# Optimization experiments

Measured on AMD Instinct MI355X. Metric: run time of the kernel, lower is better.

## Reference

```python
import jax, jax.numpy as jnp
import numpy as np

N_HEAD = 16
ROPE_BASE = 10000.0


def _rope_tables(T, head_dim, dtype=jnp.float32):
    inv_freq = 1.0 / (ROPE_BASE ** (jnp.arange(0, head_dim, 2, dtype=jnp.float32) / head_dim))
    t = jnp.arange(T, dtype=jnp.float32)
    freqs = t[:, None] * inv_freq[None, :]          # [T, D/2]
    emb = jnp.concatenate([freqs, freqs], axis=-1)  # [T, D]
    return jnp.cos(emb).astype(dtype), jnp.sin(emb).astype(dtype)


def _rotate_half(x):
    d = x.shape[-1] // 2
    return jnp.concatenate([-x[..., d:], x[..., :d]], axis=-1)


def setup_inputs() -> dict:
    key = jax.random.key(0)
    ks = jax.random.split(key, 5)
    B, T, C = 2, 2048, 2048
    s = 1.0 / np.sqrt(C)
    return {
        "x": jax.random.normal(ks[0], (B, T, C), dtype=jnp.float32),
        "wq": jax.random.normal(ks[1], (C, C), dtype=jnp.float32) * s,
        "wk": jax.random.normal(ks[2], (C, C), dtype=jnp.float32) * s,
        "wv": jax.random.normal(ks[3], (C, C), dtype=jnp.float32) * s,
        "wo": jax.random.normal(ks[4], (C, C), dtype=jnp.float32) * s,
    }


def reference(x, wq, wk, wv, wo):
    B, T, C = x.shape
    H = N_HEAD
    D = C // H

    def heads(y):  # [B,T,C] -> [B,H,T,D]
        return y.reshape(B, T, H, D).transpose(0, 2, 1, 3)

    q = heads(x @ wq)
    k = heads(x @ wk)
    v = heads(x @ wv)

    cos, sin = _rope_tables(T, D, x.dtype)          # [T, D]
    cos = cos[None, None, :, :]
    sin = sin[None, None, :, :]
    q = q * cos + _rotate_half(q) * sin
    k = k * cos + _rotate_half(k) * sin

    scale = 1.0 / np.sqrt(D)
    scores = jnp.einsum('bhqd,bhkd->bhqk', q, k) * scale   # [B,H,T,T]
    causal = jnp.tril(jnp.ones((T, T), dtype=bool))
    scores = jnp.where(causal[None, None, :, :], scores, jnp.finfo(scores.dtype).min)
    attn = jax.nn.softmax(scores, axis=-1)
    y = jnp.einsum('bhqk,bhkd->bhqd', attn, v)             # [B,H,T,D]
    y = y.transpose(0, 2, 1, 3).reshape(B, T, C)
    return y @ wo
```

## Files before the change

kernel.cpp:

```cpp
#include <hip/hip_runtime.h>
#include <hip/hip_bf16.h>
#include <math.h>


#define TT 2048
#define CCn 2048
#define HH 16
#define DD 128
#define MMr 4096
#define NQKV 6144

typedef __attribute__((ext_vector_type(8))) short s16x8;
typedef __attribute__((ext_vector_type(4))) short s16x4;
typedef __attribute__((ext_vector_type(4))) float f32x4;

__device__ __forceinline__ short bf16_of(float f) {
  unsigned u = __float_as_uint(f);
  unsigned r = u + 0x7fffu + ((u >> 16) & 1u);
  return (short)(r >> 16);
}
__device__ __forceinline__ float f_of_bf16(short s) {
  return __uint_as_float(((unsigned)(unsigned short)s) << 16);
}
__device__ __forceinline__ float ex2(float x) { return exp2f(x); }

__device__ __forceinline__ void lds_load16(const void* g, void* l) {
  __builtin_amdgcn_global_load_lds((__attribute__((address_space(1))) void*)g,
                                   (__attribute__((address_space(3))) void*)l,
                                   16, 0, 0);
}

__global__ __launch_bounds__(256) void k_tables(float* __restrict__ cosT,
                                                float* __restrict__ sinT) {
  int idx = blockIdx.x * 256 + threadIdx.x;
  int t = idx >> 6, i = idx & 63;
  float inv = powf(10000.0f, -(float)i * (1.0f / 64.0f));
  float f = (float)t * inv;
  cosT[idx] = cosf(f);
  sinT[idx] = sinf(f);
}

__global__ __launch_bounds__(256) void k_cast_x(const float* __restrict__ x,
                                                short* __restrict__ xb) {
  int i = blockIdx.x * 256 + threadIdx.x;
  f32x4 v = ((const f32x4*)x)[i];
  s16x4 o;
#pragma unroll
  for (int j = 0; j < 4; ++j) o[j] = bf16_of(v[j]);
  ((s16x4*)xb)[i] = o;
}

__global__ __launch_bounds__(256) void k_wtrans(const float* __restrict__ w,
                                                short* __restrict__ wt) {
  __shared__ float tile[32][33];
  int n0 = blockIdx.x * 32, k0 = blockIdx.y * 32;
  int tx = threadIdx.x & 31, ty = threadIdx.x >> 5;
#pragma unroll
  for (int j = 0; j < 4; ++j) {
    int k = ty * 4 + j;
    tile[k][tx] = w[(size_t)(k0 + k) * CCn + n0 + tx];
  }
  __syncthreads();
#pragma unroll
  for (int j = 0; j < 4; ++j) {
    int n = ty * 4 + j;
    wt[(size_t)(n0 + n) * CCn + k0 + tx] = bf16_of(tile[tx][n]);
  }
}

__global__ __launch_bounds__(256) void k_vtrans(const short* __restrict__ src,
                                                short* __restrict__ dst) {
  __shared__ short tile[32][33];
  int bh = blockIdx.y, b = bh >> 4, h = bh & 15;
  int dt = blockIdx.x & 3, tt = blockIdx.x >> 2;
  int tx = threadIdx.x & 31, ty = threadIdx.x >> 5;
  const short* sp = src + ((size_t)(b * TT + tt * 32)) * NQKV + 4096 + h * DD + dt * 32;
#pragma unroll
  for (int j = 0; j < 4; ++j) {
    int tr = ty * 4 + j;
    tile[tr][tx] = sp[(size_t)tr * NQKV + tx];
  }
  __syncthreads();
  short* dp = dst + ((size_t)(bh * DD + dt * 32)) * TT + tt * 32;
#pragma unroll
  for (int j = 0; j < 4; ++j) {
    int dr = ty * 4 + j;
    dp[(size_t)dr * TT + tx] = tile[tx][dr];
  }
}

__global__ __launch_bounds__(256) void k_rope(const short* __restrict__ qkv, int coff,
                                              const float* __restrict__ cosT,
                                              const float* __restrict__ sinT,
                                              short* __restrict__ dst, float mul) {
  int idx = blockIdx.x * 256 + threadIdx.x;
  int i4 = (idx & 15) * 4;
  int h = (idx >> 4) & 15;
  int t = (idx >> 8) & 2047;
  int b = idx >> 19;
  const short* row = qkv + ((size_t)(b * TT + t)) * NQKV + coff + h * DD;
  s16x4 v0 = *(const s16x4*)(row + i4);
  s16x4 v1 = *(const s16x4*)(row + i4 + 64);
  f32x4 c4 = *(const f32x4*)(cosT + t * 64 + i4);
  f32x4 s4 = *(const f32x4*)(sinT + t * 64 + i4);
  s16x4 o0, o1;
#pragma unroll
  for (int j = 0; j < 4; ++j) {
    float a = f_of_bf16(v0[j]), bb = f_of_bf16(v1[j]);
    o0[j] = bf16_of((a * c4[j] - bb * s4[j]) * mul);
    o1[j] = bf16_of((bb * c4[j] + a * s4[j]) * mul);
  }
  short* orow = dst + ((size_t)((b * HH + h) * TT + t)) * DD;
  *(s16x4*)(orow + i4) = o0;
  *(s16x4*)(orow + i4 + 64) = o1;
}

template <bool BF16OUT>
__global__ __launch_bounds__(512, 2) void k_gemm256(const short* __restrict__ A,
                                                    const short* __restrict__ Bt,
                                                    void* __restrict__ Cout,
                                                    int M, int N, int K) {
  __shared__ short smem[65536];
  const int tid = threadIdx.x, wid = tid >> 6, lane = tid & 63;
  const int wm = wid >> 2, wn = wid & 3;
  const int lr = lane & 15, lk = lane >> 4;
  const int swz = (lk ^ ((lr >> 1) & 3)) * 8;

  int nwg = gridDim.x, orig = blockIdx.x;
  int xcd = orig & 7, idx = orig >> 3;
  int q = nwg >> 3, rmd = nwg & 7;
  int wg = (xcd < rmd) ? (xcd * (q + 1) + idx)
                       : (rmd * (q + 1) + (xcd - rmd) * q + idx);
  const int NBM = M >> 8;
  const int m0 = (wg % NBM) * 256, n0 = (wg / NBM) * 256;

  const int ldsbase = (tid & ~63);

  auto stageHalf = [&](const short* src, int r0, int slot, int kt, int h) {
#pragma unroll
    for (int l = 0; l < 2; ++l) {
      int lin = l * 512 + tid;
      int rr = lin >> 2, cs = lin & 3;
      int cc = cs ^ ((rr >> 1) & 3);
      lds_load16(src + (size_t)(r0 + rr) * K + kt * 64 + h * 32 + cc * 8,
                 smem + slot + (l * 512 + ldsbase) * 8);
    }
  };
  f32x4 acc[8][4] = {};
  s16x8 af[4], bfr[4];

  const int nk = K >> 6;
  stageHalf(A, m0, 0, 0, 0);
  stageHalf(Bt, n0, 32768, 0, 0);
  stageHalf(A, m0, 8192, 0, 1);
  stageHalf(Bt, n0, 32768 + 8192, 0, 1);
  stageHalf(A, m0, 16384, 1, 0);
  stageHalf(Bt, n0, 32768 + 16384, 1, 0);
  asm volatile("s_waitcnt vmcnt(4)" ::: "memory");
  __builtin_amdgcn_s_barrier();

#define PHASE_MFMA(mh)                                                        \
  __builtin_amdgcn_s_setprio(1);                                              \
  _Pragma("unroll") for (int i = 0; i < 4; ++i)                               \
      _Pragma("unroll") for (int j = 0; j < 4; ++j)                           \
      acc[(mh)*4 + i][j] = __builtin_amdgcn_mfma_f32_16x16x32_bf16(           \
          af[i], bfr[j], acc[(mh)*4 + i][j], 0, 0, 0);                        \
  __builtin_amdgcn_s_setprio(0);

#define LOAD_A(mh, ks, abuf)                                                  \
  _Pragma("unroll") for (int i = 0; i < 4; ++i)                               \
      af[i] = *(const s16x8*)(smem + (abuf)*16384 + (ks)*8192 +               \
                              (wm * 128 + (mh)*64 + i * 16 + lr) * 32 + swz);
#define LOAD_B(ks, abuf)                                                      \
  _Pragma("unroll") for (int j = 0; j < 4; ++j)                               \
      bfr[j] = *(const s16x8*)(smem + 32768 + (abuf)*16384 + (ks)*8192 +      \
                               (wn * 64 + j * 16 + lr) * 32 + swz);

#pragma unroll 1
  for (int kt = 0; kt < nk; ++kt) {
    const int buf = kt & 1, nbuf = buf ^ 1;
    const bool s1 = (kt + 1 < nk), s2 = (kt + 2 < nk);
    LOAD_B(0, buf);
    LOAD_A(0, 0, buf);
    if (s1) stageHalf(A, m0, nbuf * 16384 + 8192, kt + 1, 1);
    __builtin_amdgcn_s_barrier();
    PHASE_MFMA(0);
    __builtin_amdgcn_s_barrier();
    LOAD_A(1, 0, buf);
    if (s1) stageHalf(Bt, n0, 32768 + nbuf * 16384 + 8192, kt + 1, 1);
    __builtin_amdgcn_s_barrier();
    PHASE_MFMA(1);
    __builtin_amdgcn_s_barrier();
    LOAD_B(1, buf);
    LOAD_A(0, 1, buf);
    if (s2) stageHalf(A, m0, buf * 16384, kt + 2, 0);
    __builtin_amdgcn_s_barrier();
    PHASE_MFMA(0);
    __builtin_amdgcn_s_barrier();
    LOAD_A(1, 1, buf);
    if (s2) stageHalf(Bt, n0, 32768 + buf * 16384, kt + 2, 0);
    __builtin_amdgcn_s_barrier();
    PHASE_MFMA(1);
    asm volatile("s_waitcnt vmcnt(4)" ::: "memory");
    __builtin_amdgcn_s_barrier();
  }
#undef PHASE_MFMA
#undef LOAD_A
#undef LOAD_B

#pragma unroll
  for (int fi = 0; fi < 8; ++fi)
#pragma unroll
    for (int j = 0; j < 4; ++j) {
      int row = m0 + wm * 128 + (fi >> 2) * 64 + (fi & 3) * 16 + lk * 4;
      int col = n0 + wn * 64 + j * 16 + lr;
#pragma unroll
      for (int rr = 0; rr < 4; ++rr) {
        if (BF16OUT)
          ((short*)Cout)[(size_t)(row + rr) * N + col] = bf16_of(acc[fi][j][rr]);
        else
          ((float*)Cout)[(size_t)(row + rr) * N + col] = acc[fi][j][rr];
      }
    }
}

__global__ __launch_bounds__(256) void k_attn(const short* __restrict__ Qb,
                                              const short* __restrict__ Kb,
                                              const short* __restrict__ Vt,
                                              short* __restrict__ yb) {
  __shared__ short Ks[2][64 * 128];
  __shared__ short Vs[128 * 64];
  __shared__ short Ps[4][16 * 72];
  const int tid = threadIdx.x, wid = tid >> 6, lane = tid & 63;
  const int lr = lane & 15, lk = lane >> 4;
  const int bh = blockIdx.y, bx = blockIdx.x;
  const size_t baseQK = (size_t)bh * TT * DD;
  const int b = bh >> 4, h = bh & 15;

  auto stageK = [&](int bi, int kt2) {
#pragma unroll
    for (int it = 0; it < 4; ++it) {
      int ch = it * 256 + tid;
      int r = ch >> 4, cc = ch & 15;
      int cs = cc ^ (r & 7);
      lds_load16(Kb + baseQK + (size_t)(kt2 * 64 + r) * DD + cs * 8,
                 &Ks[bi][(size_t)(it * 256 + wid * 64) * 8]);
    }
  };
  auto stageV = [&](int kt2) {
#pragma unroll
    for (int it = 0; it < 4; ++it) {
      int ch = it * 256 + tid;
      int d = ch >> 3, kc = ch & 7;
      int cs = kc ^ (d & 7);
      lds_load16(Vt + baseQK + (size_t)d * TT + kt2 * 64 + cs * 8,
                 &Vs[(size_t)(it * 256 + wid * 64) * 8]);
    }
  };

#pragma unroll 1
  for (int pass = 0; pass < 2; ++pass) {
    const int qt = pass ? (31 - bx) : bx;
    const int q0 = qt * 64;
    const int qg = q0 + wid * 16 + lr;
    s16x8 qf[4];
#pragma unroll
    for (int ds = 0; ds < 4; ++ds)
      qf[ds] = *(const s16x8*)(Qb + baseQK + (size_t)qg * DD + (ds * 4 + lk) * 8);

    float mrun = -3.0e38f, lrun = 0.f;
    f32x4 yacc[8] = {};

    const int nkt = qt + 1;
    stageK(0, 0);
    stageV(0);
    __syncthreads();
    int buf = 0;
#pragma unroll 1
    for (int kt = 0; kt < nkt; ++kt) {
      if (kt + 1 < nkt) stageK(buf ^ 1, kt + 1);
      f32x4 sf[4] = {};
#pragma unroll
      for (int sub = 0; sub < 4; ++sub) {
        int kr = sub * 16 + lr;
#pragma unroll
        for (int ds = 0; ds < 4; ++ds) {
          int cc = (ds * 4 + lk) ^ (kr & 7);
          s16x8 kf = *(const s16x8*)(&Ks[buf][kr * 128 + cc * 8]);
          sf[sub] = __builtin_amdgcn_mfma_f32_16x16x32_bf16(kf, qf[ds], sf[sub], 0, 0, 0);
        }
      }
      const int kvbase = kt * 64;
      if (kvbase + 63 > q0 + wid * 16) {
#pragma unroll
        for (int sub = 0; sub < 4; ++sub)
#pragma unroll
          for (int r = 0; r < 4; ++r) {
            int kv = kvbase + sub * 16 + lk * 4 + r;
            if (kv > qg) sf[sub][r] = -3.0e38f;
          }
      }
      float tmax = -3.0e38f;
#pragma unroll
      for (int sub = 0; sub < 4; ++sub)
#pragma unroll
        for (int r = 0; r < 4; ++r) tmax = fmaxf(tmax, sf[sub][r]);
      tmax = fmaxf(tmax, __shfl_xor(tmax, 16, 64));
      tmax = fmaxf(tmax, __shfl_xor(tmax, 32, 64));
      if (!__all(tmax <= mrun + 11.0f)) {
        float mnew = fmaxf(mrun, tmax);
        float alpha = ex2(mrun - mnew);
        mrun = mnew;
        lrun *= alpha;
        float ar[4];
#pragma unroll
        for (int r = 0; r < 4; ++r) ar[r] = __shfl(alpha, lk * 4 + r, 64);
#pragma unroll
        for (int dn = 0; dn < 8; ++dn)
#pragma unroll
          for (int r = 0; r < 4; ++r) yacc[dn][r] *= ar[r];
      }
      float psum = 0.f;
#pragma unroll
      for (int sub = 0; sub < 4; ++sub) {
        s16x4 pq;
#pragma unroll
        for (int r = 0; r < 4; ++r) {
          float p = ex2(sf[sub][r] - mrun);
          psum += p;
          pq[r] = bf16_of(p);
        }
        *(s16x4*)(&Ps[wid][lr * 72 + sub * 16 + lk * 4]) = pq;
      }
      psum += __shfl_xor(psum, 16, 64);
      psum += __shfl_xor(psum, 32, 64);
      lrun += psum;
      __syncthreads();
      s16x8 pf0 = *(const s16x8*)(&Ps[wid][lr * 72 + lk * 8]);
      s16x8 pf1 = *(const s16x8*)(&Ps[wid][lr * 72 + 32 + lk * 8]);
#pragma unroll
      for (int dn = 0; dn < 8; ++dn) {
        int d = dn * 16 + lr;
        s16x8 vf0 = *(const s16x8*)(&Vs[d * 64 + (lk ^ (d & 7)) * 8]);
        yacc[dn] = __builtin_amdgcn_mfma_f32_16x16x32_bf16(pf0, vf0, yacc[dn], 0, 0, 0);
        s16x8 vf1 = *(const s16x8*)(&Vs[d * 64 + ((4 + lk) ^ (d & 7)) * 8]);
        yacc[dn] = __builtin_amdgcn_mfma_f32_16x16x32_bf16(pf1, vf1, yacc[dn], 0, 0, 0);
      }
      __syncthreads();
      if (kt + 1 < nkt) stageV(kt + 1);
      buf ^= 1;
    }
    float linv = 1.f / lrun;
    float lr4[4];
#pragma unroll
    for (int r = 0; r < 4; ++r) lr4[r] = __shfl(linv, lk * 4 + r, 64);
#pragma unroll
    for (int dn = 0; dn < 8; ++dn)
#pragma unroll
      for (int r = 0; r < 4; ++r) {
        int t = q0 + wid * 16 + lk * 4 + r;
        int c = h * DD + dn * 16 + lr;
        yb[((size_t)(b * TT + t)) * CCn + c] = bf16_of(yacc[dn][r] * lr4[r]);
      }
  }
}

extern "C" void kernel_launch(void* const* d_in, const int* in_sizes, int n_in,
                              void* d_out, int out_size, void* d_ws, size_t ws_size,
                              hipStream_t stream) {
  const float* x = (const float*)d_in[0];
  const float* wq = (const float*)d_in[1];
  const float* wk = (const float*)d_in[2];
  const float* wv = (const float*)d_in[3];
  const float* wo = (const float*)d_in[4];
  float* out = (float*)d_out;
  char* ws = (char*)d_ws;

  short* xb = (short*)(ws + 0);
  short* wqkvT = (short*)(ws + 16777216);
  short* woT = (short*)(ws + 41943040);
  short* qkv = (short*)(ws + 50331648);
  short* yb = (short*)(ws + 50331648);
  short* Qb = (short*)(ws + 100663296);
  short* Kb = (short*)(ws + 117440512);
  short* Vt = (short*)(ws + 134217728);
  float* cosT = (float*)(ws + 150994944);
  float* sinT = (float*)(ws + 151519232);

  const float kmul = 1.4426950408889634f / sqrtf(128.0f);

  k_tables<<<512, 256, 0, stream>>>(cosT, sinT);
  k_cast_x<<<8192, 256, 0, stream>>>(x, xb);
  k_wtrans<<<dim3(64, 64), 256, 0, stream>>>(wq, wqkvT);
  k_wtrans<<<dim3(64, 64), 256, 0, stream>>>(wk, wqkvT + (size_t)2048 * 2048);
  k_wtrans<<<dim3(64, 64), 256, 0, stream>>>(wv, wqkvT + (size_t)4096 * 2048);
  k_wtrans<<<dim3(64, 64), 256, 0, stream>>>(wo, woT);

  k_gemm256<true><<<16 * 24, 512, 0, stream>>>(xb, wqkvT, qkv, MMr, NQKV, CCn);

  k_rope<<<4096, 256, 0, stream>>>(qkv, 0, cosT, sinT, Qb, 1.0f);
  k_rope<<<4096, 256, 0, stream>>>(qkv, 2048, cosT, sinT, Kb, kmul);
  k_vtrans<<<dim3(256, 32), 256, 0, stream>>>(qkv, Vt);

  k_attn<<<dim3(16, 32), 256, 0, stream>>>(Qb, Kb, Vt, yb);

  k_gemm256<false><<<16 * 8, 512, 0, stream>>>(yb, woT, out, MMr, CCn, CCn);
}
```

Measured before the change: 425.9 us.

## Retile GEMMs to 128xBN blocks and merge weight-transpose and rope launches

Replaces the 256x256 GEMM tile with a templated 128-row by BN-column tile: 128x384 for the QKV projection and 128x256 for the output projection. This raises the workgroup count from 384/128 to 512/256 so the GPU's CUs are better filled, at the cost of less data reuse per block. It also fuses the four weight-transpose launches into one 3D-grid launch and the two rope launches into one, to cut launch overhead. The per-block LDS footprint and register count change, which alters occupancy.

```diff
diff --git a/kernel.cpp b/kernel.cpp
--- a/kernel.cpp
+++ b/kernel.cpp
@@ -50,9 +50,16 @@
   ((s16x4*)xb)[i] = o;
 }
 
-__global__ __launch_bounds__(256) void k_wtrans(const float* __restrict__ w,
-                                                short* __restrict__ wt) {
+__global__ __launch_bounds__(256) void k_wtrans4(const float* __restrict__ w0,
+                                                 const float* __restrict__ w1,
+                                                 const float* __restrict__ w2,
+                                                 const float* __restrict__ w3,
+                                                 short* __restrict__ wqkvT,
+                                                 short* __restrict__ woT) {
   __shared__ float tile[32][33];
+  int z = blockIdx.z;
+  const float* w = (z == 0) ? w0 : (z == 1) ? w1 : (z == 2) ? w2 : w3;
+  short* wt = (z == 3) ? woT : wqkvT + (size_t)z * 2048 * 2048;
   int n0 = blockIdx.x * 32, k0 = blockIdx.y * 32;
   int tx = threadIdx.x & 31, ty = threadIdx.x >> 5;
 #pragma unroll
@@ -89,10 +96,15 @@
   }
 }
 
-__global__ __launch_bounds__(256) void k_rope(const short* __restrict__ qkv, int coff,
-                                              const float* __restrict__ cosT,
-                                              const float* __restrict__ sinT,
-                                              short* __restrict__ dst, float mul) {
+__global__ __launch_bounds__(256) void k_rope2(const short* __restrict__ qkv,
+                                               const float* __restrict__ cosT,
+                                               const float* __restrict__ sinT,
+                                               short* __restrict__ Qb,
+                                               short* __restrict__ Kb, float kmul) {
+  int which = blockIdx.y;
+  int coff = which << 11;
+  short* dstb = which ? Kb : Qb;
+  float mul = which ? kmul : 1.0f;
   int idx = blockIdx.x * 256 + threadIdx.x;
   int i4 = (idx & 15) * 4;
   int h = (idx >> 4) & 15;
@@ -110,116 +122,134 @@
     o0[j] = bf16_of((a * c4[j] - bb * s4[j]) * mul);
     o1[j] = bf16_of((bb * c4[j] + a * s4[j]) * mul);
   }
-  short* orow = dst + ((size_t)((b * HH + h) * TT + t)) * DD;
+  short* orow = dstb + ((size_t)((b * HH + h) * TT + t)) * DD;
   *(s16x4*)(orow + i4) = o0;
   *(s16x4*)(orow + i4 + 64) = o1;
 }
 
-template <bool BF16OUT>
-__global__ __launch_bounds__(512, 2) void k_gemm256(const short* __restrict__ A,
-                                                    const short* __restrict__ Bt,
-                                                    void* __restrict__ Cout,
-                                                    int M, int N, int K) {
-  __shared__ short smem[65536];
+template <int BF, int BSTG, bool BF16OUT>
+__global__ __launch_bounds__(512) void k_gemmW(const short* __restrict__ A,
+                                               const short* __restrict__ Bt,
+                                               void* __restrict__ Cout,
+                                               int M, int N, int K) {
+  constexpr int BN = BF * 64;
+  constexpr int AH = 4096;
+  constexpr int BH = BN * 32;
+  __shared__ short smem[4 * AH + 4 * BH];
   const int tid = threadIdx.x, wid = tid >> 6, lane = tid & 63;
   const int wm = wid >> 2, wn = wid & 3;
   const int lr = lane & 15, lk = lane >> 4;
   const int swz = (lk ^ ((lr >> 1) & 3)) * 8;
 
   int nwg = gridDim.x, orig = blockIdx.x;
-  int xcd = orig & 7, idx = orig >> 3;
+  int xcd = orig & 7, bidx = orig >> 3;
   int q = nwg >> 3, rmd = nwg & 7;
-  int wg = (xcd < rmd) ? (xcd * (q + 1) + idx)
-                       : (rmd * (q + 1) + (xcd - rmd) * q + idx);
-  const int NBM = M >> 8;
-  const int m0 = (wg % NBM) * 256, n0 = (wg / NBM) * 256;
-
-  const int ldsbase = (tid & ~63);
-
-  auto stageHalf = [&](const short* src, int r0, int slot, int kt, int h) {
-#pragma unroll
-    for (int l = 0; l < 2; ++l) {
+  int wg = (xcd < rmd) ? (xcd * (q + 1) + bidx)
+                       : (rmd * (q + 1) + (xcd - rmd) * q + bidx);
+  const int NBM = M >> 7;
+  const int m0 = (wg % NBM) * 128, n0 = (wg / NBM) * BN;
+
+  const int ldswave = (tid & ~63) * 8;
+
+  auto stageA = [&](int buf, int h, int kt) {
+    int rr = tid >> 2, cs = tid & 3;
+    int cc = cs ^ ((rr >> 1) & 3);
+    lds_load16(A + (size_t)(m0 + rr) * K + kt * 64 + h * 32 + cc * 8,
+               smem + buf * 2 * AH + h * AH + ldswave);
+  };
+  auto stageB = [&](int buf, int h, int kt) {
+#pragma unroll
+    for (int l = 0; l < BSTG; ++l) {
       int lin = l * 512 + tid;
       int rr = lin >> 2, cs = lin & 3;
       int cc = cs ^ ((rr >> 1) & 3);
-      lds_load16(src + (size_t)(r0 + rr) * K + kt * 64 + h * 32 + cc * 8,
-                 smem + slot + (l * 512 + ldsbase) * 8);
+      lds_load16(Bt + (size_t)(n0 + rr) * K + kt * 64 + h * 32 + cc * 8,
+                 smem + 4 * AH + buf * 2 * BH + h * BH + l * 4096 + ldswave);
     }
   };
-  f32x4 acc[8][4] = {};
-  s16x8 af[4], bfr[4];
+
+  s16x8 af[4], bfr[BF / 2];
+  f32x4 acc[4][BF] = {};
+
+#define LOAD_A(ks, buf)                                                        \
+  _Pragma("unroll") for (int i = 0; i < 4; ++i) af[i] =                        \
+      *(const s16x8*)(smem + (buf) * 2 * AH + (ks) * AH +                      \
+                      (wm * 64 + i * 16 + lr) * 32 + swz);
+#define LOAD_B(ks, bh, buf)                                                    \
+  _Pragma("unroll") for (int j = 0; j < BF / 2; ++j) bfr[j] =                  \
+      *(const s16x8*)(smem + 4 * AH + (buf) * 2 * BH + (ks) * BH +             \
+                      (wn * (BF * 16) + ((bh) * (BF / 2) + j) * 16 + lr) * 32 +\
+                      swz);
+#define PHASE_MFMA(bh)                                                         \
+  __builtin_amdgcn_s_setprio(1);                                               \
+  _Pragma("unroll") for (int i = 0; i < 4; ++i)                                \
+      _Pragma("unroll") for (int j = 0; j < BF / 2; ++j)                       \
+      acc[i][(bh) * (BF / 2) + j] = __builtin_amdgcn_mfma_f32_16x16x32_bf16(   \
+          af[i], bfr[j], acc[i][(bh) * (BF / 2) + j], 0, 0, 0);                \
+  __builtin_amdgcn_s_setprio(0);
+#define VMCNT_N()                                                              \
+  if constexpr (BSTG == 3) asm volatile("s_waitcnt vmcnt(4)" ::: "memory");    \
+  else asm volatile("s_waitcnt vmcnt(3)" ::: "memory");
 
   const int nk = K >> 6;
-  stageHalf(A, m0, 0, 0, 0);
-  stageHalf(Bt, n0, 32768, 0, 0);
-  stageHalf(A, m0, 8192, 0, 1);
-  stageHalf(Bt, n0, 32768 + 8192, 0, 1);
-  stageHalf(A, m0, 16384, 1, 0);
-  stageHalf(Bt, n0, 32768 + 16384, 1, 0);
-  asm volatile("s_waitcnt vmcnt(4)" ::: "memory");
+  stageA(0, 0, 0);
+  stageB(0, 0, 0);
+  stageA(0, 1, 0);
+  stageB(0, 1, 0);
+  stageA(1, 0, 1);
+  stageB(1, 0, 1);
+  VMCNT_N();
   __builtin_amdgcn_s_barrier();
-
-#define PHASE_MFMA(mh)                                                        \
-  __builtin_amdgcn_s_setprio(1);                                              \
-  _Pragma("unroll") for (int i = 0; i < 4; ++i)                               \
-      _Pragma("unroll") for (int j = 0; j < 4; ++j)                           \
-      acc[(mh)*4 + i][j] = __builtin_amdgcn_mfma_f32_16x16x32_bf16(           \
-          af[i], bfr[j], acc[(mh)*4 + i][j], 0, 0, 0);                        \
-  __builtin_amdgcn_s_setprio(0);
-
-#define LOAD_A(mh, ks, abuf)                                                  \
-  _Pragma("unroll") for (int i = 0; i < 4; ++i)                               \
-      af[i] = *(const s16x8*)(smem + (abuf)*16384 + (ks)*8192 +               \
-                              (wm * 128 + (mh)*64 + i * 16 + lr) * 32 + swz);
-#define LOAD_B(ks, abuf)                                                      \
-  _Pragma("unroll") for (int j = 0; j < 4; ++j)                               \
-      bfr[j] = *(const s16x8*)(smem + 32768 + (abuf)*16384 + (ks)*8192 +      \
-                               (wn * 64 + j * 16 + lr) * 32 + swz);
 
 #pragma unroll 1
   for (int kt = 0; kt < nk; ++kt) {
     const int buf = kt & 1, nbuf = buf ^ 1;
     const bool s1 = (kt + 1 < nk), s2 = (kt + 2 < nk);
-    LOAD_B(0, buf);
-    LOAD_A(0, 0, buf);
-    if (s1) stageHalf(A, m0, nbuf * 16384 + 8192, kt + 1, 1);
+    LOAD_A(0, buf);
+    LOAD_B(0, 0, buf);
+    if (s1) stageA(nbuf, 1, kt + 1);
     __builtin_amdgcn_s_barrier();
     PHASE_MFMA(0);
     __builtin_amdgcn_s_barrier();
-    LOAD_A(1, 0, buf);
-    if (s1) stageHalf(Bt, n0, 32768 + nbuf * 16384 + 8192, kt + 1, 1);
+    LOAD_B(0, 1, buf);
+    if (s1) stageB(nbuf, 1, kt + 1);
     __builtin_amdgcn_s_barrier();
     PHASE_MFMA(1);
     __builtin_amdgcn_s_barrier();
-    LOAD_B(1, buf);
-    LOAD_A(0, 1, buf);
-    if (s2) stageHalf(A, m0, buf * 16384, kt + 2, 0);
+    LOAD_A(1, buf);
+    LOAD_B(1, 0, buf);
+    if (s2) stageA(buf, 0, kt + 2);
     __builtin_amdgcn_s_barrier();
     PHASE_MFMA(0);
     __builtin_amdgcn_s_barrier();
-    LOAD_A(1, 1, buf);
-    if (s2) stageHalf(Bt, n0, 32768 + buf * 16384, kt + 2, 0);
+    LOAD_B(1, 1, buf);
+    if (s2) stageB(buf, 0, kt + 2);
     __builtin_amdgcn_s_barrier();
     PHASE_MFMA(1);
-    asm volatile("s_waitcnt vmcnt(4)" ::: "memory");
-    __builtin_amdgcn_s_barrier();
-  }
-#undef PHASE_MFMA
+    if (kt < nk - 2) {
+      VMCNT_N();
+    } else {
+      asm volatile("s_waitcnt vmcnt(0)" ::: "memory");
+    }
+    __builtin_amdgcn_s_barrier();
+  }
 #undef LOAD_A
 #undef LOAD_B
-
-#pragma unroll
-  for (int fi = 0; fi < 8; ++fi)
-#pragma unroll
-    for (int j = 0; j < 4; ++j) {
-      int row = m0 + wm * 128 + (fi >> 2) * 64 + (fi & 3) * 16 + lk * 4;
-      int col = n0 + wn * 64 + j * 16 + lr;
+#undef PHASE_MFMA
+#undef VMCNT_N
+
+#pragma unroll
+  for (int i = 0; i < 4; ++i)
+#pragma unroll
+    for (int j = 0; j < BF; ++j) {
+      int row0 = m0 + wm * 64 + i * 16 + lk * 4;
+      int col = n0 + wn * (BF * 16) + j * 16 + lr;
 #pragma unroll
       for (int rr = 0; rr < 4; ++rr) {
         if (BF16OUT)
-          ((short*)Cout)[(size_t)(row + rr) * N + col] = bf16_of(acc[fi][j][rr]);
+          ((short*)Cout)[(size_t)(row0 + rr) * N + col] = bf16_of(acc[i][j][rr]);
         else
-          ((float*)Cout)[(size_t)(row + rr) * N + col] = acc[fi][j][rr];
+          ((float*)Cout)[(size_t)(row0 + rr) * N + col] = acc[i][j][rr];
       }
     }
 }
@@ -391,18 +421,14 @@
 
   k_tables<<<512, 256, 0, stream>>>(cosT, sinT);
   k_cast_x<<<8192, 256, 0, stream>>>(x, xb);
-  k_wtrans<<<dim3(64, 64), 256, 0, stream>>>(wq, wqkvT);
-  k_wtrans<<<dim3(64, 64), 256, 0, stream>>>(wk, wqkvT + (size_t)2048 * 2048);
-  k_wtrans<<<dim3(64, 64), 256, 0, stream>>>(wv, wqkvT + (size_t)4096 * 2048);
-  k_wtrans<<<dim3(64, 64), 256, 0, stream>>>(wo, woT);
-
-  k_gemm256<true><<<16 * 24, 512, 0, stream>>>(xb, wqkvT, qkv, MMr, NQKV, CCn);
-
-  k_rope<<<4096, 256, 0, stream>>>(qkv, 0, cosT, sinT, Qb, 1.0f);
-  k_rope<<<4096, 256, 0, stream>>>(qkv, 2048, cosT, sinT, Kb, kmul);
+  k_wtrans4<<<dim3(64, 64, 4), 256, 0, stream>>>(wq, wk, wv, wo, wqkvT, woT);
+
+  k_gemmW<6, 3, true><<<512, 512, 0, stream>>>(xb, wqkvT, qkv, MMr, NQKV, CCn);
+
+  k_rope2<<<dim3(4096, 2), 256, 0, stream>>>(qkv, cosT, sinT, Qb, Kb, kmul);
   k_vtrans<<<dim3(256, 32), 256, 0, stream>>>(qkv, Vt);
 
   k_attn<<<dim3(16, 32), 256, 0, stream>>>(Qb, Kb, Vt, yb);
 
-  k_gemm256<false><<<16 * 8, 512, 0, stream>>>(yb, woT, out, MMr, CCn, CCn);
-}
+  k_gemmW<4, 2, false><<<256, 512, 0, stream>>>(yb, woT, out, MMr, CCn, CCn);
+}
```

New measurement: 401.4 us. -5.7%, faster.
